# Optimization experiments

Measured on AMD Instinct MI355X. Metric: run time of the kernel, lower is better.

The kernel has to match this reference:

```python
import jax, jax.numpy as jnp
import numpy as np

B, T, E, H = 4, 2048, 1024, 16
HD = E // H

def setup_inputs() -> dict:
    key = jax.random.key(0)
    ks = jax.random.split(key, 5)
    s = 1.0 / np.sqrt(E)
    return {
        "x": jax.random.normal(ks[0], (B, T, E), dtype=jnp.float32),
        "mask": jnp.zeros((B, T), dtype=bool),
        "qkv_w": jax.random.uniform(ks[1], (3 * E, E), jnp.float32, -s, s),
        "qkv_b": jax.random.uniform(ks[2], (3 * E,), jnp.float32, -s, s),
        "proj_w": jax.random.uniform(ks[3], (E, E), jnp.float32, -s, s),
        "proj_b": jax.random.uniform(ks[4], (E,), jnp.float32, -s, s),
    }

def reference(x, mask, qkv_w, qkv_b, proj_w, proj_b):
    b, t, e = x.shape
    qkv = x @ qkv_w.T + qkv_b                      # [b,t,3e]
    q, k, v = jnp.split(qkv, 3, axis=2)
    # [b,t,e] -> [b,h,t,hd]
    q = q.reshape(b, t, H, HD).transpose(0, 2, 1, 3)
    k = k.reshape(b, t, H, HD).transpose(0, 2, 1, 3)
    v = v.reshape(b, t, H, HD).transpose(0, 2, 1, 3)
    scale = 1.0 / np.sqrt(HD)
    attn = jnp.einsum('bhqd,bhkd->bhqk', q, k) * scale
    # mask: True -> -inf, broadcast over heads and query positions
    neg = jnp.where(mask, -jnp.inf, 0.0).astype(attn.dtype)  # [b,t]
    attn = attn + neg[:, None, None, :]
    attn = jax.nn.softmax(attn, axis=-1)
    # dropout layers in eval mode (deterministic reference)
    out = jnp.einsum('bhqk,bhkd->bhqd', attn, v)   # [b,h,t,hd]
    out = out.transpose(0, 2, 1, 3).reshape(b, t, e)
    return out @ proj_w.T + proj_b
```

## Files before the change

kernel.cpp:

```cpp
#include <hip/hip_runtime.h>
#include <stdint.h>

#define Bz  4
#define Tz  2048
#define Ez  1024
#define Hz  16
#define HDz 64
#define Mz  (Bz*Tz)

typedef short bf16x8 __attribute__((ext_vector_type(8)));
typedef float f32x4  __attribute__((ext_vector_type(4)));
typedef unsigned short u16;

__device__ __forceinline__ u16 f2bf(float f) {
  return (u16)((__builtin_bit_cast(uint32_t, f) + 0x8000u) >> 16);
}
__device__ __forceinline__ uint32_t pack2bf(float a, float b) {
  uint32_t ua = __builtin_bit_cast(uint32_t, a) + 0x8000u;
  uint32_t ub = __builtin_bit_cast(uint32_t, b) + 0x8000u;
  return __builtin_amdgcn_perm(ub, ua, 0x07060302u);
}

#if __has_builtin(__builtin_amdgcn_exp2f)
#define EXP2(x) __builtin_amdgcn_exp2f(x)
#else
#define EXP2(x) exp2f(x)
#endif

__device__ __forceinline__ void gl2lds16(const u16* g, u16* l) {
  __builtin_amdgcn_global_load_lds((const __attribute__((address_space(1))) void*)g,
                                   (__attribute__((address_space(3))) void*)l, 16, 0, 0);
}

__global__ void cvt_f32_bf16_3(const float* __restrict__ s0, u16* __restrict__ d0, int n0,
                               const float* __restrict__ s1, u16* __restrict__ d1, int n1,
                               const float* __restrict__ s2, u16* __restrict__ d2, int n2) {
  int j = blockIdx.x * blockDim.x + threadIdx.x;
  const float* s; u16* d;
  if (j < n0) { s = s0; d = d0; }
  else {
    j -= n0;
    if (j < n1) { s = s1; d = d1; }
    else { j -= n1; if (j >= n2) return; s = s2; d = d2; }
  }
  float4 f = ((const float4*)s)[j];
  uint2 o;
  o.x = pack2bf(f.x, f.y);
  o.y = pack2bf(f.z, f.w);
  ((uint2*)d)[j] = o;
}

template<int MODE>
__global__ __launch_bounds__(256, 2) void gemm_bt(
    const u16* __restrict__ A, const u16* __restrict__ Bw,
    const float* __restrict__ bias,
    u16* __restrict__ qo, u16* __restrict__ ko, u16* __restrict__ vto,
    float* __restrict__ fo)
{
  __shared__ u16 Ab[2][128*64];
  __shared__ u16 Bb[2][128*64];
  const int tid  = threadIdx.x;
  const int lane = tid & 63;
  const int wid  = tid >> 6;
  const int quad = lane >> 4;
  const int cl   = lane & 15;
  const int wm   = wid >> 1, wn = wid & 1;
  const int bm   = blockIdx.y * 128;
  const int bn   = blockIdx.x * 128;
  const int srow = lane >> 3;
  const int ssw  = lane & 7;

  f32x4 acc[4][4] = {};

  auto stage = [&](int kt, int buf) {
#pragma unroll
    for (int s = 0; s < 4; ++s) {
      const int r  = wid*32 + s*8 + srow;
      const int cc = ssw ^ (r & 7);
      gl2lds16(A + (size_t)(bm + r)*Ez + kt + cc*8, &Ab[buf][(wid*32 + s*8)*64]);
    }
#pragma unroll
    for (int s = 0; s < 4; ++s) {
      const int r  = wid*32 + s*8 + srow;
      const int cc = ssw ^ (r & 7);
      gl2lds16(Bw + (size_t)(bn + r)*Ez + kt + cc*8, &Bb[buf][(wid*32 + s*8)*64]);
    }
  };

  stage(0, 0);

#pragma unroll 2
  for (int it = 0; it < 16; ++it) {
    const int bufc = it & 1;
    __syncthreads();
    if (it < 15) stage((it+1)*64, bufc^1);
    const u16* AB = &Ab[bufc][0];
    const u16* BB = &Bb[bufc][0];
#pragma unroll
    for (int ks = 0; ks < 2; ++ks) {
      bf16x8 af[4], bfr[4];
#pragma unroll
      for (int mi = 0; mi < 4; ++mi) {
        const int row = wm*64 + mi*16 + cl;
        const int ch  = (ks*4 + quad) ^ (row & 7);
        af[mi] = *(const bf16x8*)&AB[row*64 + ch*8];
      }
#pragma unroll
      for (int ni = 0; ni < 4; ++ni) {
        const int row = wn*64 + ni*16 + cl;
        const int ch  = (ks*4 + quad) ^ (row & 7);
        bfr[ni] = *(const bf16x8*)&BB[row*64 + ch*8];
      }
#pragma unroll
      for (int mi = 0; mi < 4; ++mi)
#pragma unroll
        for (int ni = 0; ni < 4; ++ni)
          acc[mi][ni] = __builtin_amdgcn_mfma_f32_16x16x32_bf16(af[mi], bfr[ni], acc[mi][ni], 0, 0, 0);
    }
  }

  const float qsc = 0.125f * 1.4426950408889634f;
#pragma unroll
  for (int ni = 0; ni < 4; ++ni) {
    const int n   = bn + wn*64 + ni*16 + cl;
    const float bv = bias[n];
#pragma unroll
    for (int mi = 0; mi < 4; ++mi) {
      const int m0 = bm + wm*64 + mi*16 + quad*4;
      if (MODE == 0) {
        const int which = n >> 10;
        const int e = n & 1023;
        const int h = e >> 6, d = e & 63;
        const int b = m0 >> 11, t0 = m0 & 2047;
        if (which == 2) {
          uint2 pk;
          pk.x = pack2bf(acc[mi][ni][0] + bv, acc[mi][ni][1] + bv);
          pk.y = pack2bf(acc[mi][ni][2] + bv, acc[mi][ni][3] + bv);
          *(uint2*)&vto[(((size_t)(b*Hz + h))*HDz + d)*Tz + t0] = pk;
        } else {
#pragma unroll
          for (int r = 0; r < 4; ++r) {
            const int t = t0 + r;
            float val = acc[mi][ni][r] + bv;
            if (which == 0) qo[(((size_t)(b*Hz + h))*Tz + t)*HDz + d] = f2bf(val * qsc);
            else            ko[(((size_t)(b*Hz + h))*Tz + t)*HDz + d] = f2bf(val);
          }
        }
      } else {
#pragma unroll
        for (int r = 0; r < 4; ++r)
          fo[(size_t)(m0 + r)*Ez + n] = acc[mi][ni][r] + bv;
      }
    }
  }
}

__global__ __launch_bounds__(256, 4) void attn_flash(
    const u16* __restrict__ Q, const u16* __restrict__ K,
    const u16* __restrict__ Vt, const unsigned char* __restrict__ mask,
    u16* __restrict__ ctx)
{
  __shared__ u16 Kb[2][32*64];
  __shared__ u16 Vb[2][64*32];
  __shared__ u16 Pb[4*2*16*36];

  const int tid  = threadIdx.x;
  const int lane = tid & 63;
  const int wid  = tid >> 6;
  const int quad = lane >> 4;
  const int cl   = lane & 15;
  const int bh   = blockIdx.x;
  const int b    = bh >> 4;
  const int qrw  = blockIdx.y * 128 + wid * 32;
  u16* Pw = &Pb[wid * (2*16*36)];

  const int krow = wid*8  + (lane >> 3);
  const int kch  = (lane & 7) ^ (krow & 7);
  const int vrow = wid*16 + (lane >> 2);
  const int vch  = (lane & 3) ^ ((vrow >> 1) & 3);
  const u16* Kg = K  + ((size_t)bh*Tz + krow)*HDz + kch*8;
  const u16* Vg = Vt + ((size_t)bh*HDz + vrow)*Tz + vch*8;
  u16* KbL[2] = { &Kb[0][(wid*8)*64],  &Kb[1][(wid*8)*64]  };
  u16* VbL[2] = { &Vb[0][(wid*16)*32], &Vb[1][(wid*16)*32] };

  const unsigned char* mrow_p = mask + (size_t)b * Tz;
  bool domask;
  {
    const uint4* mp = (const uint4*)mrow_p;
    uint4 a = mp[lane*2], c = mp[lane*2 + 1];
    uint32_t any = a.x | a.y | a.z | a.w | c.x | c.y | c.z | c.w;
    domask = __any(any != 0);
  }

  bf16x8 aq[2][2];
#pragma unroll
  for (int qb = 0; qb < 2; ++qb) {
    const u16* Qg = Q + ((size_t)bh*Tz + qrw + qb*16 + cl)*HDz;
    aq[qb][0] = *(const bf16x8*)(Qg + quad*8);
    aq[qb][1] = *(const bf16x8*)(Qg + 32 + quad*8);
  }

  bf16x8 ones;
#pragma unroll
  for (int i = 0; i < 8; ++i) ones[i] = (short)0x3F80;

  f32x4 o[2][4] = {};
  f32x4 lacc[2] = {};

  gl2lds16(Kg, KbL[0]);
  gl2lds16(Vg, VbL[0]);

#pragma unroll 2
  for (int it = 0; it < 64; ++it) {
    const int bufc = it & 1;
    __syncthreads();
    if (it < 63) {
      gl2lds16(Kg + (size_t)(it+1)*32*HDz, KbL[bufc^1]);
      gl2lds16(Vg + (it+1)*32,             VbL[bufc^1]);
    }
    const u16* KB = &Kb[bufc][0];
    const u16* VB = &Vb[bufc][0];
    const int kt = it * 32;

    f32x4 st[2][2] = {};
#pragma unroll
    for (int kb = 0; kb < 2; ++kb) {
      bf16x8 kf[2];
#pragma unroll
      for (int nb = 0; nb < 2; ++nb) {
        const int row = nb*16 + cl;
        const int ch  = (kb*4 + quad) ^ (row & 7);
        kf[nb] = *(const bf16x8*)&KB[row*64 + ch*8];
      }
#pragma unroll
      for (int qb = 0; qb < 2; ++qb)
#pragma unroll
        for (int nb = 0; nb < 2; ++nb)
          st[qb][nb] = __builtin_amdgcn_mfma_f32_16x16x32_bf16(kf[nb], aq[qb][kb], st[qb][nb], 0, 0, 0);
    }

    if (domask) {
#pragma unroll
      for (int nb = 0; nb < 2; ++nb) {
        uint32_t mm = *(const uint32_t*)&mrow_p[kt + nb*16 + quad*4];
        if (mm) {
#pragma unroll
          for (int qb = 0; qb < 2; ++qb) {
            if (mm & 0x000000ffu) st[qb][nb][0] = -INFINITY;
            if (mm & 0x0000ff00u) st[qb][nb][1] = -INFINITY;
            if (mm & 0x00ff0000u) st[qb][nb][2] = -INFINITY;
            if (mm & 0xff000000u) st[qb][nb][3] = -INFINITY;
          }
        }
      }
    }

#pragma unroll
    for (int qb = 0; qb < 2; ++qb) {
      u16* Pq = Pw + qb * (16*36);
#pragma unroll
      for (int nb = 0; nb < 2; ++nb) {
        uint2 pk;
        pk.x = pack2bf(EXP2(st[qb][nb][0]), EXP2(st[qb][nb][1]));
        pk.y = pack2bf(EXP2(st[qb][nb][2]), EXP2(st[qb][nb][3]));
        *(uint2*)&Pq[cl*36 + (nb*4 + quad)*4] = pk;
      }
    }

    bf16x8 pf[2];
#pragma unroll
    for (int qb = 0; qb < 2; ++qb) {
      const u16* pr = &Pw[qb*(16*36) + cl*36 + quad*8];
      uint2 lo = *(const uint2*)pr;
      uint2 hi = *(const uint2*)(pr + 4);
      int4 pi = { (int)lo.x, (int)lo.y, (int)hi.x, (int)hi.y };
      pf[qb] = __builtin_bit_cast(bf16x8, pi);
      lacc[qb] = __builtin_amdgcn_mfma_f32_16x16x32_bf16(pf[qb], ones, lacc[qb], 0, 0, 0);
    }
#pragma unroll
    for (int db = 0; db < 4; ++db) {
      const int row = db*16 + cl;
      const int ch  = quad ^ ((row >> 1) & 3);
      bf16x8 bv = *(const bf16x8*)&VB[row*32 + ch*8];
#pragma unroll
      for (int qb = 0; qb < 2; ++qb)
        o[qb][db] = __builtin_amdgcn_mfma_f32_16x16x32_bf16(pf[qb], bv, o[qb][db], 0, 0, 0);
    }
  }

#pragma unroll
  for (int qb = 0; qb < 2; ++qb) {
#pragma unroll
    for (int r = 0; r < 4; ++r) {
      const float inv = 1.0f / lacc[qb][r];
      const int t = qrw + qb*16 + quad*4 + r;
      const size_t base = ((size_t)b*Tz + t)*Ez + (size_t)(bh & 15)*HDz;
#pragma unroll
      for (int db = 0; db < 4; ++db) {
        ctx[base + db*16 + cl] = f2bf(o[qb][db][r] * inv);
      }
    }
  }
}

extern "C" void kernel_launch(void* const* d_in, const int* in_sizes, int n_in,
                              void* d_out, int out_size, void* d_ws, size_t ws_size,
                              hipStream_t stream) {
  (void)in_sizes; (void)n_in; (void)out_size; (void)ws_size;
  const float* x      = (const float*)d_in[0];
  const unsigned char* mask = (const unsigned char*)d_in[1];
  const float* qkv_w  = (const float*)d_in[2];
  const float* qkv_b  = (const float*)d_in[3];
  const float* proj_w = (const float*)d_in[4];
  const float* proj_b = (const float*)d_in[5];
  float* out = (float*)d_out;

  char* ws = (char*)d_ws;
  u16* xb   = (u16*)(ws + 0);
  u16* wqb  = (u16*)(ws + 16777216);
  u16* wpb  = (u16*)(ws + 23068672);
  u16* Qb   = (u16*)(ws + 25165824);
  u16* Kb_  = (u16*)(ws + 41943040);
  u16* Vtb  = (u16*)(ws + 58720256);
  u16* ctxb = (u16*)(ws + 75497472);

  cvt_f32_bf16_3<<<12288, 256, 0, stream>>>(x, xb, 2097152,
                                            qkv_w, wqb, 786432,
                                            proj_w, wpb, 262144);

  gemm_bt<0><<<dim3(24, 64), 256, 0, stream>>>(xb, wqb, qkv_b, Qb, Kb_, Vtb, nullptr);
  attn_flash<<<dim3(64, 16), 256, 0, stream>>>(Qb, Kb_, Vtb, mask, ctxb);
  gemm_bt<1><<<dim3(8, 64), 256, 0, stream>>>(ctxb, wpb, proj_b, nullptr, nullptr, nullptr, out);
}
```

Before: 265.4 us.

## Halve GEMM K-tile to 32, raise occupancy, swap grid order for weight reuse

The GEMM K-step per stage drops from 64 to 32, which halves LDS use per block. Launch bounds rise to allow 3 blocks per CU, and the LDS XOR swizzle is reworked to fit 32-wide rows. The grid is transposed so consecutive blocks walk along M while sharing the same weight tile, which should improve L2 reuse of the B operand. The cost is twice as many barriers and fewer MFMAs per sync, and the higher occupancy target may put pressure on registers.

After: 270.6 us. About the same (+2.0%).

```diff
diff --git a/kernel.cpp b/kernel.cpp
--- a/kernel.cpp
+++ b/kernel.cpp
@@ -51,72 +51,77 @@
 }
 
 template<int MODE>
-__global__ __launch_bounds__(256, 2) void gemm_bt(
+__global__ __launch_bounds__(256, 3) void gemm_bt(
     const u16* __restrict__ A, const u16* __restrict__ Bw,
     const float* __restrict__ bias,
     u16* __restrict__ qo, u16* __restrict__ ko, u16* __restrict__ vto,
     float* __restrict__ fo)
 {
-  __shared__ u16 Ab[2][128*64];
-  __shared__ u16 Bb[2][128*64];
+  __shared__ u16 Ab[2][128*32];
+  __shared__ u16 Bb[2][128*32];
   const int tid  = threadIdx.x;
   const int lane = tid & 63;
   const int wid  = tid >> 6;
   const int quad = lane >> 4;
   const int cl   = lane & 15;
   const int wm   = wid >> 1, wn = wid & 1;
-  const int bm   = blockIdx.y * 128;
-  const int bn   = blockIdx.x * 128;
-  const int srow = lane >> 3;
-  const int ssw  = lane & 7;
+  const int bm   = blockIdx.x * 128;
+  const int bn   = blockIdx.y * 128;
+
+  const int sr = lane >> 2;
+  const int sc = lane & 3;
+  const u16* gA[2]; const u16* gB[2];
+  int ldsOff[2];
+#pragma unroll
+  for (int s = 0; s < 2; ++s) {
+    const int rl = s*64 + wid*16 + sr;
+    const int ca = sc ^ ((rl >> 1) & 3);
+    gA[s] = A  + (size_t)(bm + rl)*Ez + ca*8;
+    gB[s] = Bw + (size_t)(bn + rl)*Ez + ca*8;
+    ldsOff[s] = (s*64 + wid*16)*32;
+  }
 
   f32x4 acc[4][4] = {};
 
-  auto stage = [&](int kt, int buf) {
-#pragma unroll
-    for (int s = 0; s < 4; ++s) {
-      const int r  = wid*32 + s*8 + srow;
-      const int cc = ssw ^ (r & 7);
-      gl2lds16(A + (size_t)(bm + r)*Ez + kt + cc*8, &Ab[buf][(wid*32 + s*8)*64]);
-    }
-#pragma unroll
-    for (int s = 0; s < 4; ++s) {
-      const int r  = wid*32 + s*8 + srow;
-      const int cc = ssw ^ (r & 7);
-      gl2lds16(Bw + (size_t)(bn + r)*Ez + kt + cc*8, &Bb[buf][(wid*32 + s*8)*64]);
-    }
-  };
-
-  stage(0, 0);
+#pragma unroll
+  for (int s = 0; s < 2; ++s) {
+    gl2lds16(gA[s], &Ab[0][ldsOff[s]]);
+    gl2lds16(gB[s], &Bb[0][ldsOff[s]]);
+  }
 
 #pragma unroll 2
-  for (int it = 0; it < 16; ++it) {
+  for (int it = 0; it < 32; ++it) {
     const int bufc = it & 1;
     __syncthreads();
-    if (it < 15) stage((it+1)*64, bufc^1);
+    if (it < 31) {
+      const int kn = (it + 1) * 32;
+#pragma unroll
+      for (int s = 0; s < 2; ++s) {
+        gl2lds16(gA[s] + kn, &Ab[bufc^1][ldsOff[s]]);
+        gl2lds16(gB[s] + kn, &Bb[bufc^1][ldsOff[s]]);
+      }
+    }
     const u16* AB = &Ab[bufc][0];
     const u16* BB = &Bb[bufc][0];
-#pragma unroll
-    for (int ks = 0; ks < 2; ++ks) {
-      bf16x8 af[4], bfr[4];
-#pragma unroll
-      for (int mi = 0; mi < 4; ++mi) {
-        const int row = wm*64 + mi*16 + cl;
-        const int ch  = (ks*4 + quad) ^ (row & 7);
-        af[mi] = *(const bf16x8*)&AB[row*64 + ch*8];
-      }
-#pragma unroll
-      for (int ni = 0; ni < 4; ++ni) {
-        const int row = wn*64 + ni*16 + cl;
-        const int ch  = (ks*4 + quad) ^ (row & 7);
-        bfr[ni] = *(const bf16x8*)&BB[row*64 + ch*8];
-      }
-#pragma unroll
-      for (int mi = 0; mi < 4; ++mi)
-#pragma unroll
-        for (int ni = 0; ni < 4; ++ni)
-          acc[mi][ni] = __builtin_amdgcn_mfma_f32_16x16x32_bf16(af[mi], bfr[ni], acc[mi][ni], 0, 0, 0);
-    }
+
+    bf16x8 af[4], bfr[4];
+#pragma unroll
+    for (int mi = 0; mi < 4; ++mi) {
+      const int row = wm*64 + mi*16 + cl;
+      const int ch  = quad ^ ((row >> 1) & 3);
+      af[mi] = *(const bf16x8*)&AB[row*32 + ch*8];
+    }
+#pragma unroll
+    for (int ni = 0; ni < 4; ++ni) {
+      const int row = wn*64 + ni*16 + cl;
+      const int ch  = quad ^ ((row >> 1) & 3);
+      bfr[ni] = *(const bf16x8*)&BB[row*32 + ch*8];
+    }
+#pragma unroll
+    for (int mi = 0; mi < 4; ++mi)
+#pragma unroll
+      for (int ni = 0; ni < 4; ++ni)
+        acc[mi][ni] = __builtin_amdgcn_mfma_f32_16x16x32_bf16(af[mi], bfr[ni], acc[mi][ni], 0, 0, 0);
   }
 
   const float qsc = 0.125f * 1.4426950408889634f;
@@ -328,7 +333,7 @@
                                             qkv_w, wqb, 786432,
                                             proj_w, wpb, 262144);
 
-  gemm_bt<0><<<dim3(24, 64), 256, 0, stream>>>(xb, wqb, qkv_b, Qb, Kb_, Vtb, nullptr);
+  gemm_bt<0><<<dim3(64, 24), 256, 0, stream>>>(xb, wqb, qkv_b, Qb, Kb_, Vtb, nullptr);
   attn_flash<<<dim3(64, 16), 256, 0, stream>>>(Qb, Kb_, Vtb, mask, ctxb);
-  gemm_bt<1><<<dim3(8, 64), 256, 0, stream>>>(ctxb, wpb, proj_b, nullptr, nullptr, nullptr, out);
-}
+  gemm_bt<1><<<dim3(64, 8), 256, 0, stream>>>(ctxb, wpb, proj_b, nullptr, nullptr, nullptr, out);
+}
```
